# Performance work log

Measured on AMD Instinct MI355X. Metric: run time of the kernel, lower is better.

The kernel has to match this reference:

```python
import jax, jax.numpy as jnp
import numpy as np

B, H, M, HS = 256, 1024, 256, 128  # batch, hidden=entry_size, mem_cap, head_size
TAU = 1.0
sg = jax.lax.stop_gradient


def _gumbel(u):
    # torch: -log(1e-20 - log(1e-20 + rand))
    return -jnp.log(1e-20 - jnp.log(1e-20 + u))


def _hard_gumbel_softmax(scores, u, tau):
    # straight-through hard gumbel softmax over the memcap axis (axis=1)
    y = jax.nn.softmax((scores + sg(_gumbel(u))) * tau, axis=1)
    ymax = jnp.max(y, axis=1, keepdims=True)
    hard = (y == ymax).astype(y.dtype)
    return sg(hard - y) + y


def setup_inputs() -> dict:
    key = jax.random.key(0)
    ks = jax.random.split(key, 20)
    stdv = 1.0 / np.sqrt(H)
    U = lambda k, shp: jax.random.uniform(k, shp, jnp.float32, -stdv, stdv)
    inp = {
        'input_': jax.random.normal(ks[0], (B, H), jnp.float32),
        'h_0': jax.random.normal(ks[1], (B, H), jnp.float32),
        'mem': jnp.zeros((B, M, H), jnp.float32),
        'last_usage': jnp.full((B, M), -99999.0, jnp.float32),
        'u1': jax.random.uniform(ks[2], (B, M), jnp.float32),
        'u2': jax.random.uniform(ks[3], (B, M), jnp.float32),
        'W_ih': U(ks[4], (H, 3 * H)),
        'W_hh': U(ks[5], (H, 3 * H)),
        'W_rh': U(ks[6], (H, 3 * H)),
        'W_s1': U(ks[7], (H, H)),
        'W_s2': U(ks[8], (H, H)),
        'W_s3': U(ks[9], (H, H)),
        'bias': jnp.zeros((1, 3 * H), jnp.float32),
        'W_im': U(ks[10], (H, HS + 1)),
        'W_hm': U(ks[11], (H, HS + 1)),
        'fc1_w': U(ks[12], (HS, H)),
        'fc1_b': jnp.zeros((HS,), jnp.float32),
        'W_im1': U(ks[13], (H, HS + 1)),
        'W_hm1': U(ks[14], (H, HS + 1)),
        'W_mm1': U(ks[15], (H, HS + 1)),
        'bias_m1': jnp.zeros((1, HS + 1), jnp.float32),
        'bias_1': jnp.zeros((1, H), jnp.float32),
        'bias_2': jnp.zeros((1, H), jnp.float32),
        'bias_3': jnp.zeros((1, H), jnp.float32),
    }
    return inp


def reference(input_, h_0, mem, last_usage, u1, u2,
              W_ih, W_hh, W_rh, W_s1, W_s2, W_s3, bias,
              W_im, W_hm, fc1_w, fc1_b,
              W_im1, W_hm1, W_mm1, bias_m1, bias_1, bias_2, bias_3):
    memcap = mem.shape[1]
    hidden = h_0.shape[1]
    # write: memcnt == 0 -> one-hot write index at slot 0, broadcast over batch
    widx = jnp.zeros((1, memcap), mem.dtype).at[0, 0].set(1.0)
    ones = widx[:, :, None]                       # (1, M, 1)
    mem = h_0[:, None, :] * ones + mem * (1.0 - ones)  # (B, M, E)
    last_use = jax.nn.sigmoid(sg(last_usage))     # (B, M), detached
    # addressing head (computed on detached input/h_0/mem, as in torch)
    read_head = jnp.tanh(sg(input_) @ W_im + sg(h_0) @ W_hm)          # (B, HS+1)
    head_vecs = jnp.concatenate(
        [sg(mem) @ fc1_w.T + fc1_b, last_use[:, :, None]], axis=2)    # (B, M, HS+1)
    scores = jnp.einsum('bh,bmh->bm', read_head, head_vecs)
    y1 = _hard_gumbel_softmax(scores, u1, TAU)
    entry = jnp.einsum('bm,bme->be', y1, mem)     # (B, E)
    # GRU-like gating
    w_b = jax.nn.sigmoid(entry @ W_rh + h_0 @ W_hh + input_ @ W_ih + bias)
    r, z, n = jnp.split(w_b, 3, axis=1)
    h_new = jnp.tanh(input_ @ W_s1 + bias_1 + r * (h_0 @ W_s2 + bias_2)
                     + z * (bias_3 + entry @ W_s3))
    # second read head (not detached)
    head1 = jnp.tanh(input_ @ W_im1 + h_0 @ W_hm1 + entry @ W_mm1 + bias_m1)
    scores1 = jnp.einsum('bh,bmh->bm', head1, head_vecs)
    y2 = _hard_gumbel_softmax(scores1, u2, TAU)
    entry_o = jnp.einsum('bm,bme->be', y2, mem)
    h_1 = n * h_new + (1.0 - n) * h_0
    o = jnp.concatenate([h_1, entry_o], axis=1)
    return (h_1, o)
```

## Files before the change

### kernel.cpp

```cpp
#include <hip/hip_runtime.h>

#define BB 256
#define HH 1024
#define MM 256
#define HS 128
#define NH 129

typedef __attribute__((ext_vector_type(8))) short short8;
typedef __attribute__((ext_vector_type(4))) float float4v;

__device__ __forceinline__ float sigmoidf_(float x) { return 1.0f / (1.0f + expf(-x)); }
__device__ __forceinline__ float gumbelf_(float u) { return -logf(1e-20f - logf(1e-20f + u)); }

__device__ __forceinline__ unsigned short f2bf(float x) {
    union { float f; unsigned u; } c; c.f = x;
    unsigned u = c.u;
    return (unsigned short)((u + 0x7FFFu + ((u >> 16) & 1u)) >> 16);
}

__device__ __forceinline__ void score_from_P(const float* __restrict__ P,
                                             const float* __restrict__ sj,
                                             const float* __restrict__ sv,
                                             const float* __restrict__ h0row,
                                             float cb, float hf,
                                             const float* __restrict__ last_usage,
                                             const float* __restrict__ u,
                                             float* __restrict__ sg_out,
                                             int b, int t) {
    int wave = t >> 6, lane = t & 63;
    int mrow = wave * 16 + (lane >> 2);
    int q4 = lane & 3;
    const float* Prow = P + ((size_t)b * MM + mrow) * HS + q4 * 32;
    float p = 0.f;
#pragma unroll
    for (int g = 0; g < 8; ++g) {
        float4 pv = *(const float4*)(Prow + g * 4);
        float4 sjv = *(const float4*)(sj + q4 * 32 + g * 4);
        p += pv.x * sjv.x + pv.y * sjv.y + pv.z * sjv.z + pv.w * sjv.w;
    }
    p += __shfl_down(p, 2, 64);
    p += __shfl_down(p, 1, 64);
    if (q4 == 0 && mrow != 0) {
        int mb = b * MM + mrow;
        sg_out[mb] = p + cb + hf * sigmoidf_(last_usage[mb]) + gumbelf_(u[mb]);
    }
    if (wave == 15) {
        float q = 0.f;
#pragma unroll
        for (int it = 0; it < 4; ++it) {
            float4 mv = *(const float4*)(h0row + it * 256 + lane * 4);
            float4 rv = *(const float4*)(sv + it * 256 + lane * 4);
            q += mv.x * rv.x + mv.y * rv.y + mv.z * rv.z + mv.w * rv.w;
        }
        for (int off = 32; off > 0; off >>= 1) q += __shfl_down(q, off, 64);
        if (lane == 0) {
            int mb = b * MM;
            sg_out[mb] = q + cb + hf * sigmoidf_(last_usage[mb]) + gumbelf_(u[mb]);
        }
    }
}

__global__ __launch_bounds__(256) void k_pgemm_cvt(const float* __restrict__ mem,
                                                   const float* __restrict__ fc1_w,
                                                   const float* __restrict__ W_ih,
                                                   const float* __restrict__ W_hh,
                                                   const float* __restrict__ W_rh,
                                                   const float* __restrict__ W_s1,
                                                   const float* __restrict__ W_s2,
                                                   const float* __restrict__ W_s3,
                                                   unsigned short* __restrict__ WtG,
                                                   unsigned short* __restrict__ WtS,
                                                   float* __restrict__ P) {
    __shared__ __align__(16) unsigned char smem[73728];
    int bx = blockIdx.x, t = threadIdx.x;
    if (bx >= 512) {
        unsigned short (*T)[66] = (unsigned short (*)[66])smem;
        int tile = bx - 512;
        const float* src;
        unsigned short* dst;
        int k0, n0, sstr, dstr, krel;
        if (tile < 2304) {
            int kt = tile / 48, nt = tile % 48;
            k0 = kt * 64; n0 = nt * 64;
            src = (k0 < 1024) ? W_ih : (k0 < 2048) ? W_hh : W_rh;
            krel = k0 & 1023;
            dst = WtG; sstr = 3072; dstr = 3072;
        } else {
            int r = tile - 2304;
            int seg = r >> 8;
            int rem = r & 255;
            int kt = rem >> 4, nt = rem & 15;
            k0 = kt * 64; n0 = nt * 64;
            src = (seg == 0) ? W_s1 : (seg == 1) ? W_s2 : W_s3;
            krel = k0;
            dst = WtS + (size_t)seg * 1048576; sstr = 1024; dstr = 1024;
        }
        for (int i = 0; i < 4; ++i) {
            int e = i * 256 + t;
            int kk = e >> 4, nn0 = (e & 15) * 4;
            float4 v = *(const float4*)(src + (size_t)(krel + kk) * sstr + n0 + nn0);
            T[nn0 + 0][kk] = f2bf(v.x);
            T[nn0 + 1][kk] = f2bf(v.y);
            T[nn0 + 2][kk] = f2bf(v.z);
            T[nn0 + 3][kk] = f2bf(v.w);
        }
        __syncthreads();
        for (int i = 0; i < 8; ++i) {
            int e = i * 256 + t;
            int nn = e >> 5, kk2 = (e & 31) * 2;
            unsigned val = (unsigned)T[nn][kk2] | ((unsigned)T[nn][kk2 + 1] << 16);
            *(unsigned*)(dst + (size_t)(n0 + nn) * dstr + k0 + kk2) = val;
        }
        return;
    }
    unsigned short* As = (unsigned short*)smem;
    unsigned short* Bs = As + 128 * 72;
    int m0 = bx * 128;
    const float* Asrc = mem + (size_t)m0 * 1024;

    int wave = t >> 6, lane = t & 63;
    int wm = wave >> 1, wn = wave & 1;
    int q = lane >> 4, lm = lane & 15;

    float4v acc[4][4];
    for (int i = 0; i < 4; ++i)
        for (int j = 0; j < 4; ++j)
            acc[i][j] = (float4v){0.f, 0.f, 0.f, 0.f};

    for (int kt = 0; kt < 1024; kt += 64) {
        for (int g = 0; g < 4; ++g) {
            int gi = g * 256 + t;
            int row = gi >> 3, seg = gi & 7;
            const float* sa = Asrc + (size_t)row * 1024 + kt + seg * 8;
            float4 f0 = *(const float4*)sa;
            float4 f1 = *(const float4*)(sa + 4);
            uint4 pk;
            pk.x = (unsigned)f2bf(f0.x) | ((unsigned)f2bf(f0.y) << 16);
            pk.y = (unsigned)f2bf(f0.z) | ((unsigned)f2bf(f0.w) << 16);
            pk.z = (unsigned)f2bf(f1.x) | ((unsigned)f2bf(f1.y) << 16);
            pk.w = (unsigned)f2bf(f1.z) | ((unsigned)f2bf(f1.w) << 16);
            *(uint4*)&As[row * 72 + seg * 8] = pk;
            const float* sb = fc1_w + (size_t)row * 1024 + kt + seg * 8;
            float4 g0 = *(const float4*)sb;
            float4 g1 = *(const float4*)(sb + 4);
            uint4 qk;
            qk.x = (unsigned)f2bf(g0.x) | ((unsigned)f2bf(g0.y) << 16);
            qk.y = (unsigned)f2bf(g0.z) | ((unsigned)f2bf(g0.w) << 16);
            qk.z = (unsigned)f2bf(g1.x) | ((unsigned)f2bf(g1.y) << 16);
            qk.w = (unsigned)f2bf(g1.z) | ((unsigned)f2bf(g1.w) << 16);
            *(uint4*)&Bs[row * 72 + seg * 8] = qk;
        }
        __syncthreads();
        for (int ks = 0; ks < 64; ks += 32) {
            short8 av[4], bv[4];
            for (int i = 0; i < 4; ++i)
                av[i] = *(const short8*)&As[(wm * 64 + i * 16 + lm) * 72 + ks + q * 8];
            for (int j = 0; j < 4; ++j)
                bv[j] = *(const short8*)&Bs[(wn * 64 + j * 16 + lm) * 72 + ks + q * 8];
            for (int i = 0; i < 4; ++i)
                for (int j = 0; j < 4; ++j)
                    acc[i][j] = __builtin_amdgcn_mfma_f32_16x16x32_bf16(av[i], bv[j], acc[i][j], 0, 0, 0);
        }
        __syncthreads();
    }

    for (int i = 0; i < 4; ++i)
        for (int j = 0; j < 4; ++j) {
            int n = wn * 64 + j * 16 + lm;
            for (int reg = 0; reg < 4; ++reg) {
                int m = m0 + wm * 64 + i * 16 + q * 4 + reg;
                P[(size_t)m * HS + n] = acc[i][j][reg];
            }
        }
}

__global__ __launch_bounds__(1024) void k_score1(const float* __restrict__ input_,
                                                 const float* __restrict__ h0,
                                                 const float* __restrict__ W_im,
                                                 const float* __restrict__ W_hm,
                                                 const float* __restrict__ fc1_w,
                                                 const float* __restrict__ fc1_b,
                                                 const float* __restrict__ P,
                                                 const float* __restrict__ last_usage,
                                                 const float* __restrict__ u1,
                                                 unsigned short* __restrict__ Abf,
                                                 float* __restrict__ sg_out) {
    __shared__ __align__(16) float sx[HH];
    __shared__ __align__(16) float sh[HH];
    __shared__ __align__(16) float sv[HH];
    __shared__ float red[8][128];
    __shared__ float red2[8];
    __shared__ __align__(16) float sj[132];
    __shared__ float scb;
    int b = blockIdx.x, t = threadIdx.x;
    if (t < 256) {
        float4 v = *(const float4*)(input_ + (size_t)b * HH + t * 4);
        *(float4*)(sx + t * 4) = v;
        ushort4 o; o.x = f2bf(v.x); o.y = f2bf(v.y); o.z = f2bf(v.z); o.w = f2bf(v.w);
        *(ushort4*)(Abf + (size_t)b * 3072 + t * 4) = o;
    } else if (t < 512) {
        int tt = t - 256;
        float4 v = *(const float4*)(h0 + (size_t)b * HH + tt * 4);
        *(float4*)(sh + tt * 4) = v;
        ushort4 o; o.x = f2bf(v.x); o.y = f2bf(v.y); o.z = f2bf(v.z); o.w = f2bf(v.w);
        *(ushort4*)(Abf + (size_t)b * 3072 + 1024 + tt * 4) = o;
    }
    __syncthreads();
    {
        int j = t & 127, ks = t >> 7;
        int hb = ks * 128;
        float p = 0.f;
#pragma unroll 8
        for (int h = hb; h < hb + 128; ++h)
            p += sx[h] * W_im[h * NH + j] + sh[h] * W_hm[h * NH + j];
        red[ks][j] = p;
        if (t >= 1016) {
            int k2 = t - 1016;
            int hb2 = k2 * 128;
            float q = 0.f;
#pragma unroll 8
            for (int h = hb2; h < hb2 + 128; ++h)
                q += sx[h] * W_im[h * NH + 128] + sh[h] * W_hm[h * NH + 128];
            red2[k2] = q;
        }
    }
    __syncthreads();
    if (t < 128) {
        float s = 0.f;
        for (int k = 0; k < 8; ++k) s += red[k][t];
        sj[t] = tanhf(s);
    } else if (t == 128) {
        float s = 0.f;
        for (int k = 0; k < 8; ++k) s += red2[k];
        sj[128] = tanhf(s);
    }
    __syncthreads();
    {
        float acc = 0.f;
#pragma unroll 4
        for (int j = 0; j < HS; ++j) acc += sj[j] * fc1_w[(size_t)j * HH + t];
        sv[t] = acc;
    }
    if (t < 64) {
        float p = sj[t] * fc1_b[t] + sj[t + 64] * fc1_b[t + 64];
        for (int off = 32; off > 0; off >>= 1) p += __shfl_down(p, off, 64);
        if (t == 0) scb = p;
    }
    __syncthreads();
    score_from_P(P, sj, sv, h0 + (size_t)b * HH, scb, sj[128], last_usage, u1, sg_out, b, t);
}

__global__ __launch_bounds__(1024) void k_sel_score2(const float* __restrict__ sg1,
                                                     const float* __restrict__ mem,
                                                     const float* __restrict__ h0,
                                                     const float* __restrict__ input_,
                                                     const float* __restrict__ W_im1,
                                                     const float* __restrict__ W_hm1,
                                                     const float* __restrict__ W_mm1,
                                                     const float* __restrict__ bias_m1,
                                                     const float* __restrict__ fc1_w,
                                                     const float* __restrict__ fc1_b,
                                                     const float* __restrict__ P,
                                                     const float* __restrict__ last_usage,
                                                     const float* __restrict__ u2,
                                                     unsigned short* __restrict__ Abf,
                                                     float* __restrict__ sg_out) {
    __shared__ float svals[256];
    __shared__ int sidx[256];
    __shared__ __align__(16) float sx[HH];
    __shared__ __align__(16) float sh[HH];
    __shared__ __align__(16) float se[HH];
    __shared__ __align__(16) float sv[HH];
    __shared__ float red[8][128];
    __shared__ float red2[8];
    __shared__ __align__(16) float sj[132];
    __shared__ float scb;
    int b = blockIdx.x, t = threadIdx.x;
    if (t < 256) {
        svals[t] = sg1[b * MM + t];
        sidx[t] = t;
    }
    __syncthreads();
    for (int s = 128; s > 0; s >>= 1) {
        if (t < s) {
            if (svals[t + s] > svals[t]) { svals[t] = svals[t + s]; sidx[t] = sidx[t + s]; }
        }
        __syncthreads();
    }
    int mstar = sidx[0];
    const float* erow = (mstar == 0) ? (h0 + (size_t)b * HH) : (mem + ((size_t)(b * MM + mstar)) * HH);
    if (t < 256) {
        float4 v = *(const float4*)(erow + t * 4);
        *(float4*)(se + t * 4) = v;
        ushort4 o; o.x = f2bf(v.x); o.y = f2bf(v.y); o.z = f2bf(v.z); o.w = f2bf(v.w);
        *(ushort4*)(Abf + (size_t)b * 3072 + 2048 + t * 4) = o;
    } else if (t < 512) {
        int tt = t - 256;
        *(float4*)(sx + tt * 4) = *(const float4*)(input_ + (size_t)b * HH + tt * 4);
    } else if (t < 768) {
        int tt = t - 512;
        *(float4*)(sh + tt * 4) = *(const float4*)(h0 + (size_t)b * HH + tt * 4);
    }
    __syncthreads();
    {
        int j = t & 127, ks = t >> 7;
        int hb = ks * 128;
        float p = 0.f;
#pragma unroll 4
        for (int h = hb; h < hb + 128; ++h)
            p += sx[h] * W_im1[h * NH + j] + sh[h] * W_hm1[h * NH + j] + se[h] * W_mm1[h * NH + j];
        red[ks][j] = p;
        if (t >= 1016) {
            int k2 = t - 1016;
            int hb2 = k2 * 128;
            float q = 0.f;
#pragma unroll 4
            for (int h = hb2; h < hb2 + 128; ++h)
                q += sx[h] * W_im1[h * NH + 128] + sh[h] * W_hm1[h * NH + 128] + se[h] * W_mm1[h * NH + 128];
            red2[k2] = q;
        }
    }
    __syncthreads();
    if (t < 128) {
        float s = bias_m1[t];
        for (int k = 0; k < 8; ++k) s += red[k][t];
        sj[t] = tanhf(s);
    } else if (t == 128) {
        float s = bias_m1[128];
        for (int k = 0; k < 8; ++k) s += red2[k];
        sj[128] = tanhf(s);
    }
    __syncthreads();
    {
        float acc = 0.f;
#pragma unroll 4
        for (int j = 0; j < HS; ++j) acc += sj[j] * fc1_w[(size_t)j * HH + t];
        sv[t] = acc;
    }
    if (t < 64) {
        float p = sj[t] * fc1_b[t] + sj[t + 64] * fc1_b[t + 64];
        for (int off = 32; off > 0; off >>= 1) p += __shfl_down(p, off, 64);
        if (t == 0) scb = p;
    }
    __syncthreads();
    score_from_P(P, sj, sv, h0 + (size_t)b * HH, scb, sj[128], last_usage, u2, sg_out, b, t);
}

__global__ __launch_bounds__(256) void k_gemm(const unsigned short* __restrict__ Abf,
                                              const unsigned short* __restrict__ WtG,
                                              const unsigned short* __restrict__ WtS,
                                              float* __restrict__ wbp,
                                              float* __restrict__ Sp) {
    __shared__ unsigned short As[128 * 72];
    __shared__ unsigned short Bs[128 * 72];
    int bx = blockIdx.x;
    int mtile = bx & 1, unit = bx >> 1;
    int m0 = mtile * 128;
    const unsigned short* Bp;
    const unsigned short* Ap;
    float* pout;
    int bstr, ncol0;
    if (unit < 144) {
        int nt = unit % 24;
        int kidx = unit / 24;
        int ksel = kidx >> 1, khalf = kidx & 1;
        ncol0 = nt * 128;
        Bp = WtG + (size_t)ncol0 * 3072 + ksel * 1024 + khalf * 512;
        bstr = 3072;
        Ap = Abf + ksel * 1024 + khalf * 512;
        pout = wbp + (size_t)kidx * 786432;
    } else {
        int su = unit - 144;
        int seg = su / 16;
        int rem = su % 16;
        int khalf = rem >> 3, nts = rem & 7;
        ncol0 = seg * 1024 + nts * 128;
        Bp = WtS + (size_t)seg * 1048576 + (size_t)(nts * 128) * 1024 + khalf * 512;
        bstr = 1024;
        Ap = Abf + seg * 1024 + khalf * 512;
        pout = Sp + (size_t)khalf * 786432;
    }

    int tid = threadIdx.x;
    int wave = tid >> 6, lane = tid & 63;
    int wm = wave >> 1, wn = wave & 1;
    int q = lane >> 4, lm = lane & 15;

    float4v acc[4][4];
    for (int i = 0; i < 4; ++i)
        for (int j = 0; j < 4; ++j)
            acc[i][j] = (float4v){0.f, 0.f, 0.f, 0.f};

    for (int kt = 0; kt < 512; kt += 64) {
        for (int rr = 0; rr < 4; ++rr) {
            int e = rr * 256 + tid;
            int row = e >> 3, cg = e & 7;
            *(uint4*)&As[row * 72 + cg * 8] =
                *(const uint4*)(Ap + (size_t)(m0 + row) * 3072 + kt + cg * 8);
            *(uint4*)&Bs[row * 72 + cg * 8] =
                *(const uint4*)(Bp + (size_t)row * bstr + kt + cg * 8);
        }
        __syncthreads();
        for (int ks = 0; ks < 64; ks += 32) {
            short8 av[4], bv[4];
            for (int i = 0; i < 4; ++i)
                av[i] = *(const short8*)&As[(wm * 64 + i * 16 + lm) * 72 + ks + q * 8];
            for (int j = 0; j < 4; ++j)
                bv[j] = *(const short8*)&Bs[(wn * 64 + j * 16 + lm) * 72 + ks + q * 8];
            for (int i = 0; i < 4; ++i)
                for (int j = 0; j < 4; ++j)
                    acc[i][j] = __builtin_amdgcn_mfma_f32_16x16x32_bf16(av[i], bv[j], acc[i][j], 0, 0, 0);
        }
        __syncthreads();
    }

    for (int i = 0; i < 4; ++i)
        for (int j = 0; j < 4; ++j) {
            int n = ncol0 + wn * 64 + j * 16 + lm;
            for (int reg = 0; reg < 4; ++reg) {
                int m = m0 + wm * 64 + i * 16 + q * 4 + reg;
                pout[(size_t)m * 3072 + n] = acc[i][j][reg];
            }
        }
}

__global__ __launch_bounds__(256) void k_final(const float* __restrict__ sg2,
                                               const float* __restrict__ mem,
                                               const float* __restrict__ wbp,
                                               const float* __restrict__ Sp,
                                               const float* __restrict__ h0,
                                               const float* __restrict__ bias,
                                               const float* __restrict__ b1,
                                               const float* __restrict__ b2,
                                               const float* __restrict__ b3,
                                               float* __restrict__ out) {
    __shared__ float svals[256];
    __shared__ int sidx[256];
    int b = blockIdx.x, t = threadIdx.x;
    svals[t] = sg2[b * MM + t];
    sidx[t] = t;
    __syncthreads();
    for (int s = 128; s > 0; s >>= 1) {
        if (t < s) {
            if (svals[t + s] > svals[t]) { svals[t] = svals[t + s]; sidx[t] = sidx[t + s]; }
        }
        __syncthreads();
    }
    int mstar = sidx[0];
    const float* erow = (mstar == 0) ? (h0 + (size_t)b * HH) : (mem + ((size_t)(b * MM + mstar)) * HH);
    float* o_row = out + (size_t)BB * HH + (size_t)b * 2 * HH;
    {
        int hb = t * 4;
        *(float4*)(o_row + HH + hb) = *(const float4*)(erow + hb);
    }
    int h = t * 4;
    size_t base = (size_t)b * 3072;
    float4 wsum[3];
#pragma unroll
    for (int g = 0; g < 3; ++g) {
        float4 a = make_float4(0.f, 0.f, 0.f, 0.f);
#pragma unroll
        for (int p = 0; p < 6; ++p) {
            float4 w = *(const float4*)(wbp + (size_t)p * 786432 + base + g * 1024 + h);
            a.x += w.x; a.y += w.y; a.z += w.z; a.w += w.w;
        }
        wsum[g] = a;
    }
    float4 bi0 = *(const float4*)(bias + h);
    float4 bi1 = *(const float4*)(bias + 1024 + h);
    float4 bi2 = *(const float4*)(bias + 2048 + h);
    float4 r4 = make_float4(sigmoidf_(wsum[0].x + bi0.x), sigmoidf_(wsum[0].y + bi0.y),
                            sigmoidf_(wsum[0].z + bi0.z), sigmoidf_(wsum[0].w + bi0.w));
    float4 z4 = make_float4(sigmoidf_(wsum[1].x + bi1.x), sigmoidf_(wsum[1].y + bi1.y),
                            sigmoidf_(wsum[1].z + bi1.z), sigmoidf_(wsum[1].w + bi1.w));
    float4 n4 = make_float4(sigmoidf_(wsum[2].x + bi2.x), sigmoidf_(wsum[2].y + bi2.y),
                            sigmoidf_(wsum[2].z + bi2.z), sigmoidf_(wsum[2].w + bi2.w));
    float4 s1, s2, s3;
    {
        float4 a0 = *(const float4*)(Sp + base + h);
        float4 a1 = *(const float4*)(Sp + 786432 + base + h);
        s1 = make_float4(a0.x + a1.x, a0.y + a1.y, a0.z + a1.z, a0.w + a1.w);
        a0 = *(const float4*)(Sp + base + 1024 + h);
        a1 = *(const float4*)(Sp + 786432 + base + 1024 + h);
        s2 = make_float4(a0.x + a1.x, a0.y + a1.y, a0.z + a1.z, a0.w + a1.w);
        a0 = *(const float4*)(Sp + base + 2048 + h);
        a1 = *(const float4*)(Sp + 786432 + base + 2048 + h);
        s3 = make_float4(a0.x + a1.x, a0.y + a1.y, a0.z + a1.z, a0.w + a1.w);
    }
    float4 v1 = *(const float4*)(b1 + h);
    float4 v2 = *(const float4*)(b2 + h);
    float4 v3 = *(const float4*)(b3 + h);
    float4 h0v = *(const float4*)(h0 + (size_t)b * HH + h);
    float4 hn, h1;
    hn.x = tanhf(s1.x + v1.x + r4.x * (s2.x + v2.x) + z4.x * (s3.x + v3.x));
    hn.y = tanhf(s1.y + v1.y + r4.y * (s2.y + v2.y) + z4.y * (s3.y + v3.y));
    hn.z = tanhf(s1.z + v1.z + r4.z * (s2.z + v2.z) + z4.z * (s3.z + v3.z));
    hn.w = tanhf(s1.w + v1.w + r4.w * (s2.w + v2.w) + z4.w * (s3.w + v3.w));
    h1.x = n4.x * hn.x + (1.f - n4.x) * h0v.x;
    h1.y = n4.y * hn.y + (1.f - n4.y) * h0v.y;
    h1.z = n4.z * hn.z + (1.f - n4.z) * h0v.z;
    h1.w = n4.w * hn.w + (1.f - n4.w) * h0v.w;
    *(float4*)(out + (size_t)b * HH + h) = h1;
    *(float4*)(o_row + h) = h1;
}

extern "C" void kernel_launch(void* const* d_in, const int* in_sizes, int n_in,
                              void* d_out, int out_size, void* d_ws, size_t ws_size,
                              hipStream_t stream) {
    const float* input_ = (const float*)d_in[0];
    const float* h0 = (const float*)d_in[1];
    const float* mem = (const float*)d_in[2];
    const float* last_usage = (const float*)d_in[3];
    const float* u1 = (const float*)d_in[4];
    const float* u2 = (const float*)d_in[5];
    const float* W_ih = (const float*)d_in[6];
    const float* W_hh = (const float*)d_in[7];
    const float* W_rh = (const float*)d_in[8];
    const float* W_s1 = (const float*)d_in[9];
    const float* W_s2 = (const float*)d_in[10];
    const float* W_s3 = (const float*)d_in[11];
    const float* bias = (const float*)d_in[12];
    const float* W_im = (const float*)d_in[13];
    const float* W_hm = (const float*)d_in[14];
    const float* fc1_w = (const float*)d_in[15];
    const float* fc1_b = (const float*)d_in[16];
    const float* W_im1 = (const float*)d_in[17];
    const float* W_hm1 = (const float*)d_in[18];
    const float* W_mm1 = (const float*)d_in[19];
    const float* bias_m1 = (const float*)d_in[20];
    const float* bias_1 = (const float*)d_in[21];
    const float* bias_2 = (const float*)d_in[22];
    const float* bias_3 = (const float*)d_in[23];
    float* out = (float*)d_out;

    float* ws = (float*)d_ws;
    float* sg1 = ws;
    float* sg2 = sg1 + 65536;
    float* wbp = sg2 + 65536;
    float* Sp = wbp + 6 * 786432;
    unsigned short* Abf = (unsigned short*)(Sp + 2 * 786432);
    unsigned short* WtG = Abf + 786432;
    unsigned short* WtS = WtG + 9437184;
    float* Pbuf = (float*)(WtS + 3145728);

    k_pgemm_cvt<<<512 + 3072, 256, 0, stream>>>(mem, fc1_w, W_ih, W_hh, W_rh,
                                                W_s1, W_s2, W_s3, WtG, WtS, Pbuf);
    k_score1<<<BB, 1024, 0, stream>>>(input_, h0, W_im, W_hm, fc1_w, fc1_b,
                                      Pbuf, last_usage, u1, Abf, sg1);
    k_sel_score2<<<BB, 1024, 0, stream>>>(sg1, mem, h0, input_, W_im1, W_hm1, W_mm1, bias_m1,
                                          fc1_w, fc1_b, Pbuf, last_usage, u2, Abf, sg2);
    k_gemm<<<384, 256, 0, stream>>>(Abf, WtG, WtS, wbp, Sp);
    k_final<<<BB, 256, 0, stream>>>(sg2, mem, wbp, Sp, h0, bias, bias_1, bias_2, bias_3, out);
}
```

Baseline: 579.7 us.

## Overlap input/h0 GEMM units with selection kernel and store P in bf16

Moves the bf16 conversion of input_ and h0 into the first kernel so the GEMM units that depend only on them can run inside the selection/score2 kernel as extra blocks. The remaining entry-dependent units go to a separate GEMM kernel that now uses 1024-thread blocks with smaller per-wave tiles. P is stored in bf16 to halve its memory traffic during scoring. The cost is lower score precision from bf16 P and a different occupancy profile for the GEMM blocks.

```diff
diff --git a/kernel.cpp b/kernel.cpp
--- a/kernel.cpp
+++ b/kernel.cpp
@@ -17,8 +17,11 @@
     unsigned u = c.u;
     return (unsigned short)((u + 0x7FFFu + ((u >> 16) & 1u)) >> 16);
 }
-
-__device__ __forceinline__ void score_from_P(const float* __restrict__ P,
+__device__ __forceinline__ float bf2f(unsigned s) {
+    union { unsigned u; float f; } c; c.u = s << 16; return c.f;
+}
+
+__device__ __forceinline__ void score_from_P(const unsigned short* __restrict__ P,
                                              const float* __restrict__ sj,
                                              const float* __restrict__ sv,
                                              const float* __restrict__ h0row,
@@ -30,13 +33,17 @@
     int wave = t >> 6, lane = t & 63;
     int mrow = wave * 16 + (lane >> 2);
     int q4 = lane & 3;
-    const float* Prow = P + ((size_t)b * MM + mrow) * HS + q4 * 32;
+    const unsigned short* Prow = P + ((size_t)b * MM + mrow) * HS + q4 * 32;
     float p = 0.f;
 #pragma unroll
-    for (int g = 0; g < 8; ++g) {
-        float4 pv = *(const float4*)(Prow + g * 4);
-        float4 sjv = *(const float4*)(sj + q4 * 32 + g * 4);
-        p += pv.x * sjv.x + pv.y * sjv.y + pv.z * sjv.z + pv.w * sjv.w;
+    for (int g = 0; g < 4; ++g) {
+        uint4 pk = *(const uint4*)(Prow + g * 8);
+        float4 s0 = *(const float4*)(sj + q4 * 32 + g * 8);
+        float4 s1 = *(const float4*)(sj + q4 * 32 + g * 8 + 4);
+        p += bf2f(pk.x & 0xffffu) * s0.x + bf2f(pk.x >> 16) * s0.y +
+             bf2f(pk.y & 0xffffu) * s0.z + bf2f(pk.y >> 16) * s0.w;
+        p += bf2f(pk.z & 0xffffu) * s1.x + bf2f(pk.z >> 16) * s1.y +
+             bf2f(pk.w & 0xffffu) * s1.z + bf2f(pk.w >> 16) * s1.w;
     }
     p += __shfl_down(p, 2, 64);
     p += __shfl_down(p, 1, 64);
@@ -60,8 +67,80 @@
     }
 }
 
+__device__ __forceinline__ void gemm_unit1024(const unsigned short* __restrict__ Ap,
+                                              const unsigned short* __restrict__ Bp,
+                                              int bstr, int m0, int ncol0,
+                                              float* __restrict__ pout,
+                                              unsigned short* As, unsigned short* Bs) {
+    int t = threadIdx.x;
+    int wave = t >> 6, lane = t & 63;
+    int wm = wave >> 2, wn = wave & 3;
+    int q = lane >> 4, lm = lane & 15;
+    float4v acc[2][2];
+    for (int i = 0; i < 2; ++i)
+        for (int j = 0; j < 2; ++j)
+            acc[i][j] = (float4v){0.f, 0.f, 0.f, 0.f};
+    int row = t >> 3, cg = t & 7;
+    for (int kt = 0; kt < 512; kt += 64) {
+        *(uint4*)&As[row * 72 + cg * 8] =
+            *(const uint4*)(Ap + (size_t)(m0 + row) * 3072 + kt + cg * 8);
+        *(uint4*)&Bs[row * 72 + cg * 8] =
+            *(const uint4*)(Bp + (size_t)row * bstr + kt + cg * 8);
+        __syncthreads();
+        for (int ks = 0; ks < 64; ks += 32) {
+            short8 av[2], bv[2];
+            for (int i = 0; i < 2; ++i)
+                av[i] = *(const short8*)&As[(wm * 32 + i * 16 + lm) * 72 + ks + q * 8];
+            for (int j = 0; j < 2; ++j)
+                bv[j] = *(const short8*)&Bs[(wn * 32 + j * 16 + lm) * 72 + ks + q * 8];
+            for (int i = 0; i < 2; ++i)
+                for (int j = 0; j < 2; ++j)
+                    acc[i][j] = __builtin_amdgcn_mfma_f32_16x16x32_bf16(av[i], bv[j], acc[i][j], 0, 0, 0);
+        }
+        __syncthreads();
+    }
+    for (int i = 0; i < 2; ++i)
+        for (int j = 0; j < 2; ++j) {
+            int n = ncol0 + wn * 32 + j * 16 + lm;
+            for (int reg = 0; reg < 4; ++reg) {
+                int m = m0 + wm * 32 + i * 16 + q * 4 + reg;
+                pout[(size_t)m * 3072 + n] = acc[i][j][reg];
+            }
+        }
+}
+
+__device__ __forceinline__ void decode_unit(int unit,
+                                            const unsigned short* Abf,
+                                            const unsigned short* WtG,
+                                            const unsigned short* WtS,
+                                            float* wbp, float* Sp,
+                                            const unsigned short** Ap,
+                                            const unsigned short** Bp,
+                                            int* bstr, int* ncol0, float** pout) {
+    if (unit < 144) {
+        int nt = unit % 24, kidx = unit / 24;
+        int ksel = kidx >> 1, khalf = kidx & 1;
+        *ncol0 = nt * 128;
+        *Bp = WtG + (size_t)(nt * 128) * 3072 + ksel * 1024 + khalf * 512;
+        *bstr = 3072;
+        *Ap = Abf + ksel * 1024 + khalf * 512;
+        *pout = wbp + (size_t)kidx * 786432;
+    } else {
+        int su = unit - 144;
+        int seg = su / 16, rem = su % 16;
+        int khalf = rem >> 3, nts = rem & 7;
+        *ncol0 = seg * 1024 + nts * 128;
+        *Bp = WtS + (size_t)seg * 1048576 + (size_t)(nts * 128) * 1024 + khalf * 512;
+        *bstr = 1024;
+        *Ap = Abf + seg * 1024 + khalf * 512;
+        *pout = Sp + (size_t)khalf * 786432;
+    }
+}
+
 __global__ __launch_bounds__(256) void k_pgemm_cvt(const float* __restrict__ mem,
                                                    const float* __restrict__ fc1_w,
+                                                   const float* __restrict__ input_,
+                                                   const float* __restrict__ h0,
                                                    const float* __restrict__ W_ih,
                                                    const float* __restrict__ W_hh,
                                                    const float* __restrict__ W_rh,
@@ -70,9 +149,33 @@
                                                    const float* __restrict__ W_s3,
                                                    unsigned short* __restrict__ WtG,
                                                    unsigned short* __restrict__ WtS,
-                                                   float* __restrict__ P) {
-    __shared__ __align__(16) unsigned char smem[73728];
+                                                   unsigned short* __restrict__ Abf,
+                                                   unsigned short* __restrict__ P) {
+    __shared__ __align__(16) unsigned char smem[36864];
     int bx = blockIdx.x, t = threadIdx.x;
+    if (bx >= 3584) {
+        int tile = bx - 3584;
+        for (int g = 0; g < 4; ++g) {
+            int e4 = tile * 1024 + g * 256 + t;
+            int base = e4 * 4;
+            const float* src;
+            unsigned short* dst;
+            if (base < 262144) {
+                int b = base >> 10, pos = base & 1023;
+                src = input_ + (size_t)b * HH + pos;
+                dst = Abf + (size_t)b * 3072 + pos;
+            } else {
+                int e2 = base - 262144;
+                int b = e2 >> 10, pos = e2 & 1023;
+                src = h0 + (size_t)b * HH + pos;
+                dst = Abf + (size_t)b * 3072 + 1024 + pos;
+            }
+            float4 v = *(const float4*)src;
+            ushort4 o; o.x = f2bf(v.x); o.y = f2bf(v.y); o.z = f2bf(v.z); o.w = f2bf(v.w);
+            *(ushort4*)dst = o;
+        }
+        return;
+    }
     if (bx >= 512) {
         unsigned short (*T)[66] = (unsigned short (*)[66])smem;
         int tile = bx - 512;
@@ -169,7 +272,7 @@
             int n = wn * 64 + j * 16 + lm;
             for (int reg = 0; reg < 4; ++reg) {
                 int m = m0 + wm * 64 + i * 16 + q * 4 + reg;
-                P[(size_t)m * HS + n] = acc[i][j][reg];
+                P[(size_t)m * HS + n] = f2bf(acc[i][j][reg]);
             }
         }
 }
@@ -180,10 +283,9 @@
                                                  const float* __restrict__ W_hm,
                                                  const float* __restrict__ fc1_w,
                                                  const float* __restrict__ fc1_b,
-                                                 const float* __restrict__ P,
+                                                 const unsigned short* __restrict__ P,
                                                  const float* __restrict__ last_usage,
                                                  const float* __restrict__ u1,
-                                                 unsigned short* __restrict__ Abf,
                                                  float* __restrict__ sg_out) {
     __shared__ __align__(16) float sx[HH];
     __shared__ __align__(16) float sh[HH];
@@ -194,16 +296,10 @@
     __shared__ float scb;
     int b = blockIdx.x, t = threadIdx.x;
     if (t < 256) {
-        float4 v = *(const float4*)(input_ + (size_t)b * HH + t * 4);
-        *(float4*)(sx + t * 4) = v;
-        ushort4 o; o.x = f2bf(v.x); o.y = f2bf(v.y); o.z = f2bf(v.z); o.w = f2bf(v.w);
-        *(ushort4*)(Abf + (size_t)b * 3072 + t * 4) = o;
+        *(float4*)(sx + t * 4) = *(const float4*)(input_ + (size_t)b * HH + t * 4);
     } else if (t < 512) {
         int tt = t - 256;
-        float4 v = *(const float4*)(h0 + (size_t)b * HH + tt * 4);
-        *(float4*)(sh + tt * 4) = v;
-        ushort4 o; o.x = f2bf(v.x); o.y = f2bf(v.y); o.z = f2bf(v.z); o.w = f2bf(v.w);
-        *(ushort4*)(Abf + (size_t)b * 3072 + 1024 + tt * 4) = o;
+        *(float4*)(sh + tt * 4) = *(const float4*)(h0 + (size_t)b * HH + tt * 4);
     }
     __syncthreads();
     {
@@ -250,32 +346,51 @@
     score_from_P(P, sj, sv, h0 + (size_t)b * HH, scb, sj[128], last_usage, u1, sg_out, b, t);
 }
 
-__global__ __launch_bounds__(1024) void k_sel_score2(const float* __restrict__ sg1,
-                                                     const float* __restrict__ mem,
-                                                     const float* __restrict__ h0,
-                                                     const float* __restrict__ input_,
-                                                     const float* __restrict__ W_im1,
-                                                     const float* __restrict__ W_hm1,
-                                                     const float* __restrict__ W_mm1,
-                                                     const float* __restrict__ bias_m1,
-                                                     const float* __restrict__ fc1_w,
-                                                     const float* __restrict__ fc1_b,
-                                                     const float* __restrict__ P,
-                                                     const float* __restrict__ last_usage,
-                                                     const float* __restrict__ u2,
-                                                     unsigned short* __restrict__ Abf,
-                                                     float* __restrict__ sg_out) {
-    __shared__ float svals[256];
-    __shared__ int sidx[256];
-    __shared__ __align__(16) float sx[HH];
-    __shared__ __align__(16) float sh[HH];
-    __shared__ __align__(16) float se[HH];
-    __shared__ __align__(16) float sv[HH];
-    __shared__ float red[8][128];
-    __shared__ float red2[8];
-    __shared__ __align__(16) float sj[132];
-    __shared__ float scb;
-    int b = blockIdx.x, t = threadIdx.x;
+__global__ __launch_bounds__(1024) void k_sel_gemm(const float* __restrict__ sg1,
+                                                   const float* __restrict__ mem,
+                                                   const float* __restrict__ h0,
+                                                   const float* __restrict__ input_,
+                                                   const float* __restrict__ W_im1,
+                                                   const float* __restrict__ W_hm1,
+                                                   const float* __restrict__ W_mm1,
+                                                   const float* __restrict__ bias_m1,
+                                                   const float* __restrict__ fc1_w,
+                                                   const float* __restrict__ fc1_b,
+                                                   const unsigned short* __restrict__ P,
+                                                   const float* __restrict__ last_usage,
+                                                   const float* __restrict__ u2,
+                                                   unsigned short* __restrict__ Abf,
+                                                   const unsigned short* __restrict__ WtG,
+                                                   const unsigned short* __restrict__ WtS,
+                                                   float* __restrict__ wbp,
+                                                   float* __restrict__ Sp,
+                                                   float* __restrict__ sg_out) {
+    __shared__ __align__(16) unsigned char smem[36864];
+    int bx = blockIdx.x, t = threadIdx.x;
+    if (bx >= 256) {
+        int g = bx - 256;
+        int mtile = g & 1, idx = g >> 1;
+        int unit = (idx < 96) ? idx : 144 + (idx - 96);
+        const unsigned short *Ap, *Bp;
+        int bstr, ncol0;
+        float* pout;
+        decode_unit(unit, Abf, WtG, WtS, wbp, Sp, &Ap, &Bp, &bstr, &ncol0, &pout);
+        unsigned short* As = (unsigned short*)smem;
+        unsigned short* Bs = As + 128 * 72;
+        gemm_unit1024(Ap, Bp, bstr, mtile * 128, ncol0, pout, As, Bs);
+        return;
+    }
+    float* sx = (float*)smem;
+    float* sh = sx + 1024;
+    float* se = sh + 1024;
+    float* sv = se + 1024;
+    float* svals = sv + 1024;
+    int* sidx = (int*)(svals + 256);
+    float* red = (float*)(sidx + 256);
+    float* red2 = red + 1024;
+    float* sj = red2 + 8;
+    float* scb = sj + 132;
+    int b = bx;
     if (t < 256) {
         svals[t] = sg1[b * MM + t];
         sidx[t] = t;
@@ -309,7 +424,7 @@
 #pragma unroll 4
         for (int h = hb; h < hb + 128; ++h)
             p += sx[h] * W_im1[h * NH + j] + sh[h] * W_hm1[h * NH + j] + se[h] * W_mm1[h * NH + j];
-        red[ks][j] = p;
+        red[ks * 128 + j] = p;
         if (t >= 1016) {
             int k2 = t - 1016;
             int hb2 = k2 * 128;
@@ -323,7 +438,7 @@
     __syncthreads();
     if (t < 128) {
         float s = bias_m1[t];
-        for (int k = 0; k < 8; ++k) s += red[k][t];
+        for (int k = 0; k < 8; ++k) s += red[k * 128 + t];
         sj[t] = tanhf(s);
     } else if (t == 128) {
         float s = bias_m1[128];
@@ -340,88 +455,28 @@
     if (t < 64) {
         float p = sj[t] * fc1_b[t] + sj[t + 64] * fc1_b[t + 64];
         for (int off = 32; off > 0; off >>= 1) p += __shfl_down(p, off, 64);
-        if (t == 0) scb = p;
-    }
-    __syncthreads();
-    score_from_P(P, sj, sv, h0 + (size_t)b * HH, scb, sj[128], last_usage, u2, sg_out, b, t);
-}
-
-__global__ __launch_bounds__(256) void k_gemm(const unsigned short* __restrict__ Abf,
-                                              const unsigned short* __restrict__ WtG,
-                                              const unsigned short* __restrict__ WtS,
-                                              float* __restrict__ wbp,
-                                              float* __restrict__ Sp) {
-    __shared__ unsigned short As[128 * 72];
-    __shared__ unsigned short Bs[128 * 72];
+        if (t == 0) *scb = p;
+    }
+    __syncthreads();
+    score_from_P(P, sj, sv, h0 + (size_t)b * HH, *scb, sj[128], last_usage, u2, sg_out, b, t);
+}
+
+__global__ __launch_bounds__(1024) void k_gemm2(const unsigned short* __restrict__ Abf,
+                                                const unsigned short* __restrict__ WtG,
+                                                const unsigned short* __restrict__ WtS,
+                                                float* __restrict__ wbp,
+                                                float* __restrict__ Sp) {
+    __shared__ __align__(16) unsigned char smem[36864];
     int bx = blockIdx.x;
-    int mtile = bx & 1, unit = bx >> 1;
-    int m0 = mtile * 128;
-    const unsigned short* Bp;
-    const unsigned short* Ap;
+    int mtile = bx & 1, idx = bx >> 1;
+    int unit = (idx < 48) ? 96 + idx : 176 + (idx - 48);
+    const unsigned short *Ap, *Bp;
+    int bstr, ncol0;
     float* pout;
-    int bstr, ncol0;
-    if (unit < 144) {
-        int nt = unit % 24;
-        int kidx = unit / 24;
-        int ksel = kidx >> 1, khalf = kidx & 1;
-        ncol0 = nt * 128;
-        Bp = WtG + (size_t)ncol0 * 3072 + ksel * 1024 + khalf * 512;
-        bstr = 3072;
-        Ap = Abf + ksel * 1024 + khalf * 512;
-        pout = wbp + (size_t)kidx * 786432;
-    } else {
-        int su = unit - 144;
-        int seg = su / 16;
-        int rem = su % 16;
-        int khalf = rem >> 3, nts = rem & 7;
-        ncol0 = seg * 1024 + nts * 128;
-        Bp = WtS + (size_t)seg * 1048576 + (size_t)(nts * 128) * 1024 + khalf * 512;
-        bstr = 1024;
-        Ap = Abf + seg * 1024 + khalf * 512;
-        pout = Sp + (size_t)khalf * 786432;
-    }
-
-    int tid = threadIdx.x;
-    int wave = tid >> 6, lane = tid & 63;
-    int wm = wave >> 1, wn = wave & 1;
-    int q = lane >> 4, lm = lane & 15;
-
-    float4v acc[4][4];
-    for (int i = 0; i < 4; ++i)
-        for (int j = 0; j < 4; ++j)
-            acc[i][j] = (float4v){0.f, 0.f, 0.f, 0.f};
-
-    for (int kt = 0; kt < 512; kt += 64) {
-        for (int rr = 0; rr < 4; ++rr) {
-            int e = rr * 256 + tid;
-            int row = e >> 3, cg = e & 7;
-            *(uint4*)&As[row * 72 + cg * 8] =
-                *(const uint4*)(Ap + (size_t)(m0 + row) * 3072 + kt + cg * 8);
-            *(uint4*)&Bs[row * 72 + cg * 8] =
-                *(const uint4*)(Bp + (size_t)row * bstr + kt + cg * 8);
-        }
-        __syncthreads();
-        for (int ks = 0; ks < 64; ks += 32) {
-            short8 av[4], bv[4];
-            for (int i = 0; i < 4; ++i)
-                av[i] = *(const short8*)&As[(wm * 64 + i * 16 + lm) * 72 + ks + q * 8];
-            for (int j = 0; j < 4; ++j)
-                bv[j] = *(const short8*)&Bs[(wn * 64 + j * 16 + lm) * 72 + ks + q * 8];
-            for (int i = 0; i < 4; ++i)
-                for (int j = 0; j < 4; ++j)
-                    acc[i][j] = __builtin_amdgcn_mfma_f32_16x16x32_bf16(av[i], bv[j], acc[i][j], 0, 0, 0);
-        }
-        __syncthreads();
-    }
-
-    for (int i = 0; i < 4; ++i)
-        for (int j = 0; j < 4; ++j) {
-            int n = ncol0 + wn * 64 + j * 16 + lm;
-            for (int reg = 0; reg < 4; ++reg) {
-                int m = m0 + wm * 64 + i * 16 + q * 4 + reg;
-                pout[(size_t)m * 3072 + n] = acc[i][j][reg];
-            }
-        }
+    decode_unit(unit, Abf, WtG, WtS, wbp, Sp, &Ap, &Bp, &bstr, &ncol0, &pout);
+    unsigned short* As = (unsigned short*)smem;
+    unsigned short* Bs = As + 128 * 72;
+    gemm_unit1024(Ap, Bp, bstr, mtile * 128, ncol0, pout, As, Bs);
 }
 
 __global__ __launch_bounds__(256) void k_final(const float* __restrict__ sg2,
@@ -541,14 +596,15 @@
     unsigned short* Abf = (unsigned short*)(Sp + 2 * 786432);
     unsigned short* WtG = Abf + 786432;
     unsigned short* WtS = WtG + 9437184;
-    float* Pbuf = (float*)(WtS + 3145728);
-
-    k_pgemm_cvt<<<512 + 3072, 256, 0, stream>>>(mem, fc1_w, W_ih, W_hh, W_rh,
-                                                W_s1, W_s2, W_s3, WtG, WtS, Pbuf);
+    unsigned short* Pbuf = WtS + 3145728;
+
+    k_pgemm_cvt<<<3712, 256, 0, stream>>>(mem, fc1_w, input_, h0, W_ih, W_hh, W_rh,
+                                          W_s1, W_s2, W_s3, WtG, WtS, Abf, Pbuf);
     k_score1<<<BB, 1024, 0, stream>>>(input_, h0, W_im, W_hm, fc1_w, fc1_b,
-                                      Pbuf, last_usage, u1, Abf, sg1);
-    k_sel_score2<<<BB, 1024, 0, stream>>>(sg1, mem, h0, input_, W_im1, W_hm1, W_mm1, bias_m1,
-                                          fc1_w, fc1_b, Pbuf, last_usage, u2, Abf, sg2);
-    k_gemm<<<384, 256, 0, stream>>>(Abf, WtG, WtS, wbp, Sp);
+                                      Pbuf, last_usage, u1, sg1);
+    k_sel_gemm<<<512, 1024, 0, stream>>>(sg1, mem, h0, input_, W_im1, W_hm1, W_mm1, bias_m1,
+                                         fc1_w, fc1_b, Pbuf, last_usage, u2,
+                                         Abf, WtG, WtS, wbp, Sp, sg2);
+    k_gemm2<<<128, 1024, 0, stream>>>(Abf, WtG, WtS, wbp, Sp);
     k_final<<<BB, 256, 0, stream>>>(sg2, mem, wbp, Sp, h0, bias, bias_1, bias_2, bias_3, out);
 }
```

Result: no change. 575.2 us (-0.8%).
